# Kernel optimization log

Hardware: AMD Instinct MI355X
Metric: run time of the kernel (lower is better)

The kernel has to match this reference:

```python
import jax, jax.numpy as jnp
import numpy as np

VOCAB = 50000; EMBED = 300; KDIM = 128; KNUM = 21; KSIZES = (1, 2, 3)
B = 32; QLEN = 32; DLEN = 1024


def _kernel_mus(n):
    mus = [1.0]
    bs = 2.0 / (n - 1)
    mus.append(1.0 - bs / 2)
    for i in range(1, n - 1):
        mus.append(mus[i] - bs)
    return np.asarray(mus, np.float32)


def _kernel_sigmas(n):
    return np.asarray([0.001] + [0.1] * (n - 1), np.float32)


def setup_inputs() -> dict:
    key = jax.random.key(0)
    ks = jax.random.split(key, 12)
    inp = {
        'query_ids': jax.random.randint(ks[0], (B, QLEN), 0, VOCAB),
        'query_masks': jnp.ones((B, QLEN), jnp.float32),
        'doc_ids': jax.random.randint(ks[1], (B, DLEN), 0, VOCAB),
        'doc_masks': jnp.ones((B, DLEN), jnp.float32),
        'emb': jax.random.normal(ks[2], (VOCAB, EMBED), jnp.float32) * 0.02,
    }
    for i, k in enumerate(KSIZES):
        inp[f'conv_w{i+1}'] = jax.random.normal(ks[3 + i], (KDIM, EMBED, k), jnp.float32) / np.sqrt(EMBED * k)
        inp[f'conv_b{i+1}'] = jnp.zeros((KDIM,), jnp.float32)
    feat = KNUM * len(KSIZES) ** 2  # 189
    inp['dense_w'] = jax.random.normal(ks[9], (feat, 1), jnp.float32) * 0.05
    inp['dense_b'] = jnp.zeros((1,), jnp.float32)
    return inp


def _conv_relu(x, w, b):
    # x: [B, L, E], w: [O, E, K] -> [B, L-K+1, O] (VALID conv, matches torch Conv1d no padding)
    y = jax.lax.conv_general_dilated(x, w, (1,), 'VALID', dimension_numbers=('NWC', 'OIW', 'NWC'))
    return jax.nn.relu(y + b)


def _matcher(k_enc, k_mask, v_enc, v_mask, mus, sig):
    kn = k_enc / (jnp.linalg.norm(k_enc, axis=-1, keepdims=True) + 1e-13)
    vn = v_enc / (jnp.linalg.norm(v_enc, axis=-1, keepdims=True) + 1e-13)
    inter = jnp.einsum('bqd,bvd->bqv', kn, vn) * (k_mask[:, :, None] * v_mask[:, None, :])
    # multi-Gaussian soft-histogram over similarity: [B, q, v, KNUM]
    ko = jnp.exp(-((inter[..., None] - mus) ** 2) / (2.0 * sig ** 2))
    kde = jnp.log(jnp.maximum(ko.sum(axis=2), 1e-10)) * 0.01  # [B, q, KNUM]
    return (kde * k_mask[..., None]).sum(axis=1)  # [B, KNUM]


def reference(query_ids, query_masks, doc_ids, doc_masks, emb,
              conv_w1, conv_b1, conv_w2, conv_b2, conv_w3, conv_b3,
              dense_w, dense_b):
    mus = jnp.asarray(_kernel_mus(KNUM))
    sig = jnp.asarray(_kernel_sigmas(KNUM))
    qe = emb[query_ids]  # [B, QLEN, E]
    de = emb[doc_ids]    # [B, DLEN, E]
    cw = [(conv_w1, conv_b1), (conv_w2, conv_b2), (conv_w3, conv_b3)]
    q_encs = [_conv_relu(qe, w, b) for w, b in cw]
    d_encs = [_conv_relu(de, w, b) for w, b in cw]
    logits = jnp.concatenate([
        _matcher(q, query_masks[:, :q.shape[1]], d, doc_masks[:, :d.shape[1]], mus, sig)
        for q in q_encs for d in d_encs], axis=1)  # [B, 189]
    score = (logits @ dense_w + dense_b).squeeze(-1)  # [B]
    return score, logits
```

## Files before the change

### kernel.cpp

```cpp
#include <hip/hip_runtime.h>
#include <hip/hip_bf16.h>
#include <math.h>

#define NB 32
#define QL 32
#define DL 1024
#define EMB 300
#define EMBP 320
#define OD 128
#define KNUM 21
#define VOCAB 50000

typedef short short8 __attribute__((ext_vector_type(8)));
typedef float floatx4 __attribute__((ext_vector_type(4)));

static const size_t WP_OFF  = 0;
static const size_t DPK_OFF = 122880;
static const size_t QPK_OFF = 5365760;
static const size_t QH_OFF  = 5529920;
static const size_t QLO_OFF = 5726528;
static const size_t DH_OFF  = 5923136;
static const size_t DLO_OFF = 12214592;
static const size_t ACC_OFF = 18506048;
static const int ACC_SZ = 9 * NB * QL * KNUM;

#define QPLANE 131072
#define DPLANE 4194304

#define MROWS (NB * DL + NB * QL)
#define MTILES 264
#define CONV_BLOCKS (MTILES * 3)

#define PREPW_N 245760
#define GATHER_N ((MROWS + 2) * 40)

__device__ __constant__ int WPOFF_C[3] = {0, 40960, 122880};

__device__ __forceinline__ void gl_lds16(const ushort* g, char* l) {
    __builtin_amdgcn_global_load_lds(
        (const __attribute__((address_space(1))) unsigned int*)(g),
        (__attribute__((address_space(3))) unsigned int*)(l), 16, 0, 0);
}

__device__ __forceinline__ ushort bf16_bits(float f) {
    __hip_bfloat16 h = __float2bfloat16(f);
    return *reinterpret_cast<ushort*>(&h);
}

__global__ void gather_prep(const float* __restrict__ emb,
                            const int* __restrict__ dids, const int* __restrict__ qids,
                            const float* __restrict__ w1, const float* __restrict__ w2,
                            const float* __restrict__ w3,
                            ushort* __restrict__ dpk, ushort* __restrict__ qpk,
                            ushort* __restrict__ wp) {
    int idx = blockIdx.x * 256 + threadIdx.x;
    if (idx < PREPW_N) {
        const float* src;
        int k, rel, base;
        if (idx < 40960)        { k = 1; rel = idx;          src = w1; base = 0; }
        else if (idx < 122880)  { k = 2; rel = idx - 40960;  src = w2; base = 40960; }
        else                    { k = 3; rel = idx - 122880; src = w3; base = 122880; }
        int kd = 320 * k;
        int o = rel / kd;
        int jc = rel - o * kd;
        int j = jc / EMBP;
        int c = jc - j * EMBP;
        float f = (c < EMB) ? src[(o * EMB + c) * k + j] : 0.f;
        wp[base + rel] = bf16_bits(f);
        return;
    }
    idx -= PREPW_N;
    if (idx >= GATHER_N) return;
    const int DROWS = NB * DL;
    int r = idx / 40;
    int c0 = (idx - r * 40) * 8;
    int rid;
    ushort* dst;
    if (r < DROWS) { rid = dids[r]; dst = dpk + (size_t)r * EMBP; }
    else if (r < DROWS + NB * QL) { rid = qids[r - DROWS]; dst = qpk + (size_t)(r - DROWS) * EMBP; }
    else {
        uint4 zz = {0u, 0u, 0u, 0u};
        *reinterpret_cast<uint4*>(qpk + (size_t)(r - DROWS) * EMBP + c0) = zz;
        return;
    }
    const float* erow = emb + (size_t)rid * EMB;
    ushort v[8];
    if (c0 + 8 <= EMB) {
        float4 f0 = *reinterpret_cast<const float4*>(erow + c0);
        float4 f1 = *reinterpret_cast<const float4*>(erow + c0 + 4);
        float fv[8] = {f0.x, f0.y, f0.z, f0.w, f1.x, f1.y, f1.z, f1.w};
#pragma unroll
        for (int i = 0; i < 8; ++i) v[i] = bf16_bits(fv[i]);
    } else {
#pragma unroll
        for (int i = 0; i < 8; ++i) {
            int c = c0 + i;
            v[i] = bf16_bits((c < EMB) ? erow[c] : 0.f);
        }
    }
    *reinterpret_cast<uint4*>(dst + c0) = *reinterpret_cast<uint4*>(v);
}

__global__ __launch_bounds__(256) void conv_mfma(const ushort* __restrict__ xpk,
                                                 const float* __restrict__ dmask,
                                                 const float* __restrict__ qmask,
                                                 const ushort* __restrict__ wp,
                                                 const float* __restrict__ b1,
                                                 const float* __restrict__ b2,
                                                 const float* __restrict__ b3,
                                                 ushort* __restrict__ dh,
                                                 ushort* __restrict__ dlo,
                                                 ushort* __restrict__ qh,
                                                 ushort* __restrict__ qlo) {
    __shared__ __align__(16) char smem[2][33024];

    const int tid = threadIdx.x;
    const int bid = blockIdx.x;
    const int swz = (bid & 7) * (CONV_BLOCKS / 8) + (bid >> 3);
    const int z = swz % 3;
    const int tile = swz / 3;
    const int l0 = tile * 128;

    const int Kdim = EMBP * (z + 1);
    const int nk = 5 * (z + 1);
    const ushort* wpk = wp + WPOFF_C[z];
    const float* bias = (z == 0) ? b1 : ((z == 1) ? b2 : b3);

    const int wave = tid >> 6;
    const int lane = tid & 63;
    const int l15 = lane & 15;
    const int quad = lane >> 4;
    const int wm = wave >> 1;
    const int wn = wave & 1;

    const int srow = lane >> 3;
    const int scolx = (((lane & 7) ^ (lane >> 3) ^ 0) & 7) * 8;
    const ushort* a0 = xpk + (size_t)(l0 + wave * 8 + srow) * EMBP + scolx;
    const ushort* at = xpk + (size_t)(l0 + 128 + srow) * EMBP + scolx;
    const ushort* b0 = wpk + (size_t)(wave * 8 + srow) * Kdim + scolx;

    auto stage = [&](int buf, int kk) {
        int jj = (kk >= 10) ? 2 : ((kk >= 5) ? 1 : 0);
        int coff = (kk - jj * 5) * 64;
        int koff = kk * 64;
        char* abuf = smem[buf];
        char* bbuf = smem[buf] + 16640;
#pragma unroll
        for (int p = 0; p < 4; ++p)
            gl_lds16(a0 + p * (32 * EMBP) + coff, abuf + p * 4096 + wave * 1024);
        if (wave == 0 && lane < 16)
            gl_lds16(at + coff, abuf + 16384);
#pragma unroll
        for (int p = 0; p < 4; ++p)
            gl_lds16(b0 + (size_t)p * 32 * Kdim + koff, bbuf + p * 4096 + wave * 1024);
    };

    floatx4 acc[4][4];
#pragma unroll
    for (int i = 0; i < 4; ++i)
#pragma unroll
        for (int j = 0; j < 4; ++j) acc[i][j] = (floatx4)0.f;

    stage(0, 0);
    __syncthreads();

    int jjc = 0, ccc = 0;
    int buf = 0;
    for (int kk = 0; kk < nk; ++kk) {
        if (kk + 1 < nk) stage(buf ^ 1, kk + 1);
        const char* Ab = smem[buf];
        const char* Bb = smem[buf] + 16640;
        short8 af[2][4], bf[2][4];
#pragma unroll
        for (int h = 0; h < 2; ++h)
#pragma unroll
            for (int i = 0; i < 4; ++i) {
                int ra = wm * 64 + i * 16 + l15 + jjc;
                int rb = wn * 64 + i * 16 + l15;
                af[h][i] = *reinterpret_cast<const short8*>(
                    Ab + ra * 128 + ((((h << 2) | quad) ^ (ra & 7)) << 4));
                bf[h][i] = *reinterpret_cast<const short8*>(
                    Bb + rb * 128 + ((((h << 2) | quad) ^ (rb & 7)) << 4));
            }
#pragma unroll
        for (int h = 0; h < 2; ++h)
#pragma unroll
            for (int i = 0; i < 4; ++i)
#pragma unroll
                for (int j = 0; j < 4; ++j)
                    acc[i][j] = __builtin_amdgcn_mfma_f32_16x16x32_bf16(af[h][i], bf[h][j], acc[i][j], 0, 0, 0);
        ++ccc;
        if (ccc == 5) { ccc = 0; ++jjc; }
        __syncthreads();
        buf ^= 1;
    }

    float (*rowsum)[128] = reinterpret_cast<float(*)[128]>(smem);
    float bv[4];
#pragma unroll
    for (int j = 0; j < 4; ++j) bv[j] = bias[wn * 64 + j * 16 + l15];
#pragma unroll
    for (int i = 0; i < 4; ++i)
#pragma unroll
        for (int r = 0; r < 4; ++r) {
            float p = 0.f;
#pragma unroll
            for (int j = 0; j < 4; ++j) {
                float y = fmaxf(acc[i][j][r] + bv[j], 0.f);
                acc[i][j][r] = y;
                p += y * y;
            }
#pragma unroll
            for (int m = 1; m < 16; m <<= 1) p += __shfl_xor(p, m, 64);
            if (l15 == 0) rowsum[wn][wm * 64 + i * 16 + quad * 4 + r] = p;
        }
    __syncthreads();

#pragma unroll
    for (int i = 0; i < 4; ++i) {
#pragma unroll
        for (int rr = 0; rr < 4; ++rr) {
            int rl = wm * 64 + i * 16 + quad * 4 + rr;
            int r = l0 + rl;
            float tot = rowsum[0][rl] + rowsum[1][rl];
            float mv;
            ushort* hp;
            ushort* lp;
            if (r < NB * DL) {
                int l = r & (DL - 1);
                if (l >= DL - z) continue;
                mv = dmask[r];
                size_t base = (size_t)z * DPLANE + (size_t)r * OD;
                hp = dh + base; lp = dlo + base;
            } else {
                int t = r - NB * DL;
                int l = t & (QL - 1);
                if (l >= QL - z) continue;
                mv = qmask[t];
                size_t base = (size_t)z * QPLANE + (size_t)t * OD;
                hp = qh + base; lp = qlo + base;
            }
            float sc = mv / (sqrtf(tot) + 1e-13f);
            int cb = wn * 64 + l15;
#pragma unroll
            for (int j = 0; j < 4; ++j) {
                float v = acc[i][j][rr] * sc;
                __hip_bfloat16 h = __float2bfloat16(v);
                float hf = __bfloat162float(h);
                hp[cb + j * 16] = *reinterpret_cast<ushort*>(&h);
                __hip_bfloat16 l = __float2bfloat16(v - hf);
                lp[cb + j * 16] = *reinterpret_cast<ushort*>(&l);
            }
        }
    }
}

__global__ __launch_bounds__(256, 4) void matcher_kernel(const ushort* __restrict__ qh_g,
                                                         const ushort* __restrict__ ql_g,
                                                         const ushort* __restrict__ vh_g,
                                                         const ushort* __restrict__ vl_g,
                                                         float* __restrict__ accb) {
    __shared__ __align__(16) float Sm[32 * 132];
    __shared__ float stageb[672];

    const int tid = threadIdx.x;
    const int pp = blockIdx.z;
    const int b = blockIdx.y;
    const int v0 = blockIdx.x * 128;
    const int qi = pp / 3;
    const int di = pp - qi * 3;
    const int Vk = 1024 - di;

    const ushort* qhb = qh_g + (size_t)qi * QPLANE + (size_t)b * (QL * OD);
    const ushort* qlb = ql_g + (size_t)qi * QPLANE + (size_t)b * (QL * OD);
    const ushort* vhb = vh_g + (size_t)di * DPLANE + (size_t)b * (DL * OD) + (size_t)v0 * OD;
    const ushort* vlb = vl_g + (size_t)di * DPLANE + (size_t)b * (DL * OD) + (size_t)v0 * OD;

    const int wave = tid >> 6;
    const int lane = tid & 63;
    const int l15 = lane & 15;
    const int quad = lane >> 4;

    floatx4 acc[2][2];
#pragma unroll
    for (int i = 0; i < 2; ++i)
#pragma unroll
        for (int j = 0; j < 2; ++j) acc[i][j] = (floatx4)0.f;

#pragma unroll
    for (int kw = 0; kw < 4; ++kw) {
        const int ko = kw * 32 + quad * 8;
        short8 qh[2], ql[2], vh[2], vl[2];
#pragma unroll
        for (int i = 0; i < 2; ++i) {
            const int qr = i * 16 + l15;
            const int vr = wave * 32 + i * 16 + l15;
            qh[i] = *reinterpret_cast<const short8*>(qhb + qr * OD + ko);
            ql[i] = *reinterpret_cast<const short8*>(qlb + qr * OD + ko);
            vh[i] = *reinterpret_cast<const short8*>(vhb + (size_t)vr * OD + ko);
            vl[i] = *reinterpret_cast<const short8*>(vlb + (size_t)vr * OD + ko);
        }
#pragma unroll
        for (int i = 0; i < 2; ++i)
#pragma unroll
            for (int j = 0; j < 2; ++j) {
                acc[i][j] = __builtin_amdgcn_mfma_f32_16x16x32_bf16(qh[i], vh[j], acc[i][j], 0, 0, 0);
                acc[i][j] = __builtin_amdgcn_mfma_f32_16x16x32_bf16(qh[i], vl[j], acc[i][j], 0, 0, 0);
                acc[i][j] = __builtin_amdgcn_mfma_f32_16x16x32_bf16(ql[i], vh[j], acc[i][j], 0, 0, 0);
            }
    }

    const int vmax = min(128, Vk - v0);
#pragma unroll
    for (int i = 0; i < 2; ++i)
#pragma unroll
        for (int j = 0; j < 2; ++j)
#pragma unroll
            for (int r = 0; r < 4; ++r) {
                int q = i * 16 + quad * 4 + r;
                int v = wave * 32 + j * 16 + l15;
                float val = acc[i][j][r];
                if (v >= vmax) val = 1.0e4f;
                Sm[q * 132 + v] = val;
            }
    __syncthreads();

    {
        const int q = tid >> 3;
        const int c = tid & 7;
        const float* srow = &Sm[q * 132 + c * 16];
        const float Am  = -72.13475204f;
        const float Am5 = -14.426950408f;
        const float A0  = -721347.52f;
        const float C   = 0x1.0p-126f;

        float s00 = 0.f, s01 = 0.f, s02 = 0.f, s03 = 0.f, s04 = 0.f, s05 = 0.f,
              s06 = 0.f, s07 = 0.f, s08 = 0.f, s09 = 0.f, s10 = 0.f, s11 = 0.f,
              s12 = 0.f, s13 = 0.f, s14 = 0.f, s15 = 0.f, s16 = 0.f, s17 = 0.f,
              s18 = 0.f, s19 = 0.f, s20 = 0.f;

#define GACC(B) { B = __builtin_fmaf(tx, C, B); B = __builtin_fmaf(ty, C, B); \
                  B = __builtin_fmaf(tz, C, B); B = __builtin_fmaf(tw, C, B); }
#define GSTEP(B, g) { tx *= Rx * (g); ty *= Ry * (g); tz *= Rz * (g); tw *= Rw * (g); GACC(B) }

#pragma unroll
        for (int jj = 0; jj < 4; ++jj) {
            float4 s4 = *reinterpret_cast<const float4*>(srow + jj * 4);
            float dx = s4.x - 0.95f, dy = s4.y - 0.95f, dz = s4.z - 0.95f, dwv = s4.w - 0.95f;
            float tx = __builtin_exp2f(__builtin_fmaf(Am * dx, dx, 126.f));
            float ty = __builtin_exp2f(__builtin_fmaf(Am * dy, dy, 126.f));
            float tz = __builtin_exp2f(__builtin_fmaf(Am * dz, dz, 126.f));
            float tw = __builtin_exp2f(__builtin_fmaf(Am * dwv, dwv, 126.f));
            float Rx = __builtin_exp2f(Am5 * dx);
            float Ry = __builtin_exp2f(Am5 * dy);
            float Rz = __builtin_exp2f(Am5 * dz);
            float Rw = __builtin_exp2f(Am5 * dwv);
            GACC(s01)
            GSTEP(s02, 6.0653066e-01f) GSTEP(s03, 2.2313016e-01f)
            GSTEP(s04, 8.2084999e-02f) GSTEP(s05, 3.0197383e-02f)
            GSTEP(s06, 1.1108997e-02f) GSTEP(s07, 4.0867714e-03f)
            GSTEP(s08, 1.5034391e-03f) GSTEP(s09, 5.5308438e-04f)
            GSTEP(s10, 2.0346837e-04f) GSTEP(s11, 7.4851830e-05f)
            GSTEP(s12, 2.7536450e-05f) GSTEP(s13, 1.0130095e-05f)
            GSTEP(s14, 3.7266532e-06f) GSTEP(s15, 1.3709590e-06f)
            GSTEP(s16, 5.0434766e-07f) GSTEP(s17, 1.8553914e-07f)
            GSTEP(s18, 6.8256033e-08f) GSTEP(s19, 2.5110699e-08f)
            GSTEP(s20, 9.2374496e-09f)
            float ex = s4.x - 1.f, ey = s4.y - 1.f, ez = s4.z - 1.f, ew = s4.w - 1.f;
            s00 += __builtin_exp2f((A0 * ex) * ex);
            s00 += __builtin_exp2f((A0 * ey) * ey);
            s00 += __builtin_exp2f((A0 * ez) * ez);
            s00 += __builtin_exp2f((A0 * ew) * ew);
        }
#undef GSTEP
#undef GACC

#define GRED(B) { B += __shfl_xor(B, 1, 64); B += __shfl_xor(B, 2, 64); B += __shfl_xor(B, 4, 64); }
        GRED(s00) GRED(s01) GRED(s02) GRED(s03) GRED(s04) GRED(s05) GRED(s06)
        GRED(s07) GRED(s08) GRED(s09) GRED(s10) GRED(s11) GRED(s12) GRED(s13)
        GRED(s14) GRED(s15) GRED(s16) GRED(s17) GRED(s18) GRED(s19) GRED(s20)
#undef GRED
        if (c == 0) {
            float* sp = &stageb[q * KNUM];
            sp[0]  = s00; sp[1]  = s01; sp[2]  = s02; sp[3]  = s03; sp[4]  = s04;
            sp[5]  = s05; sp[6]  = s06; sp[7]  = s07; sp[8]  = s08; sp[9]  = s09;
            sp[10] = s10; sp[11] = s11; sp[12] = s12; sp[13] = s13; sp[14] = s14;
            sp[15] = s15; sp[16] = s16; sp[17] = s17; sp[18] = s18; sp[19] = s19;
            sp[20] = s20;
        }
    }
    __syncthreads();

    {
        float* dst = &accb[((size_t)(pp * NB + b) * QL) * KNUM];
        for (int i = tid; i < 32 * KNUM; i += 256)
            atomicAdd(dst + i, stageb[i]);
    }
}

__global__ void finalize_kernel(const float* __restrict__ accb,
                                const float* __restrict__ qmask,
                                const float* __restrict__ dw,
                                const float* __restrict__ db,
                                float* __restrict__ out) {
    __shared__ float prod[192];
    int b = blockIdx.x;
    int tid = threadIdx.x;
    if (tid < 189) {
        int pq = tid / 21;
        int t = tid - pq * 21;
        int qi = pq / 3;
        int Qk = 32 - qi;
        const float* ab = accb + ((pq * NB + b) * QL) * KNUM + t;
        float s = 0.f;
        for (int q = 0; q < Qk; ++q)
            s += logf(fmaxf(ab[q * KNUM], 1e-10f)) * qmask[b * QL + q];
        float lg = s * 0.01f;
        out[NB + b * 189 + tid] = lg;
        prod[tid] = lg * dw[tid];
    }
    __syncthreads();
    if (tid == 0) {
        float sc = db[0];
        for (int i = 0; i < 189; ++i) sc += prod[i];
        out[b] = sc;
    }
}

extern "C" void kernel_launch(void* const* d_in, const int* in_sizes, int n_in,
                              void* d_out, int out_size, void* d_ws, size_t ws_size,
                              hipStream_t stream) {
    const int* qids = (const int*)d_in[0];
    const float* qmask = (const float*)d_in[1];
    const int* dids = (const int*)d_in[2];
    const float* dmask = (const float*)d_in[3];
    const float* emb = (const float*)d_in[4];
    const float* w1 = (const float*)d_in[5];
    const float* b1 = (const float*)d_in[6];
    const float* w2 = (const float*)d_in[7];
    const float* b2 = (const float*)d_in[8];
    const float* w3 = (const float*)d_in[9];
    const float* b3 = (const float*)d_in[10];
    const float* dw = (const float*)d_in[11];
    const float* db = (const float*)d_in[12];
    float* out = (float*)d_out;
    float* ws = (float*)d_ws;

    ushort* wp  = (ushort*)(ws + WP_OFF);
    ushort* dpk = (ushort*)(ws + DPK_OFF);
    ushort* qpk = (ushort*)(ws + QPK_OFF);
    ushort* qh  = (ushort*)(ws + QH_OFF);
    ushort* qlo = (ushort*)(ws + QLO_OFF);
    ushort* dh  = (ushort*)(ws + DH_OFF);
    ushort* dlo = (ushort*)(ws + DLO_OFF);
    float* accb = ws + ACC_OFF;

    hipMemsetAsync(accb, 0, ACC_SZ * sizeof(float), stream);
    gather_prep<<<(PREPW_N + GATHER_N + 255) / 256, 256, 0, stream>>>(
        emb, dids, qids, w1, w2, w3, dpk, qpk, wp);

    conv_mfma<<<CONV_BLOCKS, 256, 0, stream>>>(dpk, dmask, qmask, wp, b1, b2, b3, dh, dlo, qh, qlo);

    matcher_kernel<<<dim3(8, NB, 9), 256, 0, stream>>>(qh, qlo, dh, dlo, accb);
    finalize_kernel<<<NB, 256, 0, stream>>>(accb, qmask, dw, db, out);
}
```

Measured before the change: 220.4 us.

## Reuse doc tile across all three query encodings in one matcher block

The matcher grid's z dimension now covers only the three doc encodings, and each block loops over the three query encodings. The doc high/low bf16 fragments are loaded once per k-step and reused for the MFMA against all three query planes, cutting global doc traffic to a third. The cost is three times the accumulator registers, serialized Gaussian-histogram passes inside each block, and a third as many blocks, which may reduce parallelism and latency hiding. A redundant XOR term in the conv swizzle is also removed.

```diff
diff --git a/kernel.cpp b/kernel.cpp
--- a/kernel.cpp
+++ b/kernel.cpp
@@ -134,7 +134,7 @@
     const int wn = wave & 1;
 
     const int srow = lane >> 3;
-    const int scolx = (((lane & 7) ^ (lane >> 3) ^ 0) & 7) * 8;
+    const int scolx = (((lane & 7) ^ (lane >> 3)) & 7) * 8;
     const ushort* a0 = xpk + (size_t)(l0 + wave * 8 + srow) * EMBP + scolx;
     const ushort* at = xpk + (size_t)(l0 + 128 + srow) * EMBP + scolx;
     const ushort* b0 = wpk + (size_t)(wave * 8 + srow) * Kdim + scolx;
@@ -264,15 +264,13 @@
     __shared__ float stageb[672];
 
     const int tid = threadIdx.x;
-    const int pp = blockIdx.z;
+    const int di = blockIdx.z;
     const int b = blockIdx.y;
     const int v0 = blockIdx.x * 128;
-    const int qi = pp / 3;
-    const int di = pp - qi * 3;
     const int Vk = 1024 - di;
 
-    const ushort* qhb = qh_g + (size_t)qi * QPLANE + (size_t)b * (QL * OD);
-    const ushort* qlb = ql_g + (size_t)qi * QPLANE + (size_t)b * (QL * OD);
+    const ushort* qhB = qh_g + (size_t)b * (QL * OD);
+    const ushort* qlB = ql_g + (size_t)b * (QL * OD);
     const ushort* vhb = vh_g + (size_t)di * DPLANE + (size_t)b * (DL * OD) + (size_t)v0 * OD;
     const ushort* vlb = vl_g + (size_t)di * DPLANE + (size_t)b * (DL * OD) + (size_t)v0 * OD;
 
@@ -281,120 +279,133 @@
     const int l15 = lane & 15;
     const int quad = lane >> 4;
 
-    floatx4 acc[2][2];
-#pragma unroll
-    for (int i = 0; i < 2; ++i)
-#pragma unroll
-        for (int j = 0; j < 2; ++j) acc[i][j] = (floatx4)0.f;
+    floatx4 acc[3][2][2];
+#pragma unroll
+    for (int qi = 0; qi < 3; ++qi)
+#pragma unroll
+        for (int i = 0; i < 2; ++i)
+#pragma unroll
+            for (int j = 0; j < 2; ++j) acc[qi][i][j] = (floatx4)0.f;
 
 #pragma unroll
     for (int kw = 0; kw < 4; ++kw) {
         const int ko = kw * 32 + quad * 8;
-        short8 qh[2], ql[2], vh[2], vl[2];
+        short8 vh[2], vl[2];
 #pragma unroll
         for (int i = 0; i < 2; ++i) {
-            const int qr = i * 16 + l15;
             const int vr = wave * 32 + i * 16 + l15;
-            qh[i] = *reinterpret_cast<const short8*>(qhb + qr * OD + ko);
-            ql[i] = *reinterpret_cast<const short8*>(qlb + qr * OD + ko);
             vh[i] = *reinterpret_cast<const short8*>(vhb + (size_t)vr * OD + ko);
             vl[i] = *reinterpret_cast<const short8*>(vlb + (size_t)vr * OD + ko);
         }
 #pragma unroll
+        for (int qi = 0; qi < 3; ++qi) {
+            short8 qh[2], ql[2];
+#pragma unroll
+            for (int i = 0; i < 2; ++i) {
+                const int qr = i * 16 + l15;
+                qh[i] = *reinterpret_cast<const short8*>(qhB + qi * QPLANE + qr * OD + ko);
+                ql[i] = *reinterpret_cast<const short8*>(qlB + qi * QPLANE + qr * OD + ko);
+            }
+#pragma unroll
+            for (int i = 0; i < 2; ++i)
+#pragma unroll
+                for (int j = 0; j < 2; ++j) {
+                    acc[qi][i][j] = __builtin_amdgcn_mfma_f32_16x16x32_bf16(qh[i], vh[j], acc[qi][i][j], 0, 0, 0);
+                    acc[qi][i][j] = __builtin_amdgcn_mfma_f32_16x16x32_bf16(qh[i], vl[j], acc[qi][i][j], 0, 0, 0);
+                    acc[qi][i][j] = __builtin_amdgcn_mfma_f32_16x16x32_bf16(ql[i], vh[j], acc[qi][i][j], 0, 0, 0);
+                }
+        }
+    }
+
+    const int vmax = min(128, Vk - v0);
+
+#pragma unroll
+    for (int qi = 0; qi < 3; ++qi) {
+#pragma unroll
         for (int i = 0; i < 2; ++i)
 #pragma unroll
-            for (int j = 0; j < 2; ++j) {
-                acc[i][j] = __builtin_amdgcn_mfma_f32_16x16x32_bf16(qh[i], vh[j], acc[i][j], 0, 0, 0);
-                acc[i][j] = __builtin_amdgcn_mfma_f32_16x16x32_bf16(qh[i], vl[j], acc[i][j], 0, 0, 0);
-                acc[i][j] = __builtin_amdgcn_mfma_f32_16x16x32_bf16(ql[i], vh[j], acc[i][j], 0, 0, 0);
-            }
-    }
-
-    const int vmax = min(128, Vk - v0);
-#pragma unroll
-    for (int i = 0; i < 2; ++i)
-#pragma unroll
-        for (int j = 0; j < 2; ++j)
-#pragma unroll
-            for (int r = 0; r < 4; ++r) {
-                int q = i * 16 + quad * 4 + r;
-                int v = wave * 32 + j * 16 + l15;
-                float val = acc[i][j][r];
-                if (v >= vmax) val = 1.0e4f;
-                Sm[q * 132 + v] = val;
-            }
-    __syncthreads();
-
-    {
-        const int q = tid >> 3;
-        const int c = tid & 7;
-        const float* srow = &Sm[q * 132 + c * 16];
-        const float Am  = -72.13475204f;
-        const float Am5 = -14.426950408f;
-        const float A0  = -721347.52f;
-        const float C   = 0x1.0p-126f;
-
-        float s00 = 0.f, s01 = 0.f, s02 = 0.f, s03 = 0.f, s04 = 0.f, s05 = 0.f,
-              s06 = 0.f, s07 = 0.f, s08 = 0.f, s09 = 0.f, s10 = 0.f, s11 = 0.f,
-              s12 = 0.f, s13 = 0.f, s14 = 0.f, s15 = 0.f, s16 = 0.f, s17 = 0.f,
-              s18 = 0.f, s19 = 0.f, s20 = 0.f;
+            for (int j = 0; j < 2; ++j)
+#pragma unroll
+                for (int r = 0; r < 4; ++r) {
+                    int q = i * 16 + quad * 4 + r;
+                    int v = wave * 32 + j * 16 + l15;
+                    float val = acc[qi][i][j][r];
+                    if (v >= vmax) val = 1.0e4f;
+                    Sm[q * 132 + v] = val;
+                }
+        __syncthreads();
+
+        {
+            const int q = tid >> 3;
+            const int c = tid & 7;
+            const float* srow = &Sm[q * 132 + c * 16];
+            const float Am  = -72.13475204f;
+            const float Am5 = -14.426950408f;
+            const float A0  = -721347.52f;
+            const float C   = 0x1.0p-126f;
+
+            float s00 = 0.f, s01 = 0.f, s02 = 0.f, s03 = 0.f, s04 = 0.f, s05 = 0.f,
+                  s06 = 0.f, s07 = 0.f, s08 = 0.f, s09 = 0.f, s10 = 0.f, s11 = 0.f,
+                  s12 = 0.f, s13 = 0.f, s14 = 0.f, s15 = 0.f, s16 = 0.f, s17 = 0.f,
+                  s18 = 0.f, s19 = 0.f, s20 = 0.f;
 
 #define GACC(B) { B = __builtin_fmaf(tx, C, B); B = __builtin_fmaf(ty, C, B); \
                   B = __builtin_fmaf(tz, C, B); B = __builtin_fmaf(tw, C, B); }
 #define GSTEP(B, g) { tx *= Rx * (g); ty *= Ry * (g); tz *= Rz * (g); tw *= Rw * (g); GACC(B) }
 
 #pragma unroll
-        for (int jj = 0; jj < 4; ++jj) {
-            float4 s4 = *reinterpret_cast<const float4*>(srow + jj * 4);
-            float dx = s4.x - 0.95f, dy = s4.y - 0.95f, dz = s4.z - 0.95f, dwv = s4.w - 0.95f;
-            float tx = __builtin_exp2f(__builtin_fmaf(Am * dx, dx, 126.f));
-            float ty = __builtin_exp2f(__builtin_fmaf(Am * dy, dy, 126.f));
-            float tz = __builtin_exp2f(__builtin_fmaf(Am * dz, dz, 126.f));
-            float tw = __builtin_exp2f(__builtin_fmaf(Am * dwv, dwv, 126.f));
-            float Rx = __builtin_exp2f(Am5 * dx);
-            float Ry = __builtin_exp2f(Am5 * dy);
-            float Rz = __builtin_exp2f(Am5 * dz);
-            float Rw = __builtin_exp2f(Am5 * dwv);
-            GACC(s01)
-            GSTEP(s02, 6.0653066e-01f) GSTEP(s03, 2.2313016e-01f)
-            GSTEP(s04, 8.2084999e-02f) GSTEP(s05, 3.0197383e-02f)
-            GSTEP(s06, 1.1108997e-02f) GSTEP(s07, 4.0867714e-03f)
-            GSTEP(s08, 1.5034391e-03f) GSTEP(s09, 5.5308438e-04f)
-            GSTEP(s10, 2.0346837e-04f) GSTEP(s11, 7.4851830e-05f)
-            GSTEP(s12, 2.7536450e-05f) GSTEP(s13, 1.0130095e-05f)
-            GSTEP(s14, 3.7266532e-06f) GSTEP(s15, 1.3709590e-06f)
-            GSTEP(s16, 5.0434766e-07f) GSTEP(s17, 1.8553914e-07f)
-            GSTEP(s18, 6.8256033e-08f) GSTEP(s19, 2.5110699e-08f)
-            GSTEP(s20, 9.2374496e-09f)
-            float ex = s4.x - 1.f, ey = s4.y - 1.f, ez = s4.z - 1.f, ew = s4.w - 1.f;
-            s00 += __builtin_exp2f((A0 * ex) * ex);
-            s00 += __builtin_exp2f((A0 * ey) * ey);
-            s00 += __builtin_exp2f((A0 * ez) * ez);
-            s00 += __builtin_exp2f((A0 * ew) * ew);
-        }
+            for (int jj = 0; jj < 4; ++jj) {
+                float4 s4 = *reinterpret_cast<const float4*>(srow + jj * 4);
+                float dx = s4.x - 0.95f, dy = s4.y - 0.95f, dz = s4.z - 0.95f, dwv = s4.w - 0.95f;
+                float tx = __builtin_exp2f(__builtin_fmaf(Am * dx, dx, 126.f));
+                float ty = __builtin_exp2f(__builtin_fmaf(Am * dy, dy, 126.f));
+                float tz = __builtin_exp2f(__builtin_fmaf(Am * dz, dz, 126.f));
+                float tw = __builtin_exp2f(__builtin_fmaf(Am * dwv, dwv, 126.f));
+                float Rx = __builtin_exp2f(Am5 * dx);
+                float Ry = __builtin_exp2f(Am5 * dy);
+                float Rz = __builtin_exp2f(Am5 * dz);
+                float Rw = __builtin_exp2f(Am5 * dwv);
+                GACC(s01)
+                GSTEP(s02, 6.0653066e-01f) GSTEP(s03, 2.2313016e-01f)
+                GSTEP(s04, 8.2084999e-02f) GSTEP(s05, 3.0197383e-02f)
+                GSTEP(s06, 1.1108997e-02f) GSTEP(s07, 4.0867714e-03f)
+                GSTEP(s08, 1.5034391e-03f) GSTEP(s09, 5.5308438e-04f)
+                GSTEP(s10, 2.0346837e-04f) GSTEP(s11, 7.4851830e-05f)
+                GSTEP(s12, 2.7536450e-05f) GSTEP(s13, 1.0130095e-05f)
+                GSTEP(s14, 3.7266532e-06f) GSTEP(s15, 1.3709590e-06f)
+                GSTEP(s16, 5.0434766e-07f) GSTEP(s17, 1.8553914e-07f)
+                GSTEP(s18, 6.8256033e-08f) GSTEP(s19, 2.5110699e-08f)
+                GSTEP(s20, 9.2374496e-09f)
+                float ex = s4.x - 1.f, ey = s4.y - 1.f, ez = s4.z - 1.f, ew = s4.w - 1.f;
+                s00 += __builtin_exp2f((A0 * ex) * ex);
+                s00 += __builtin_exp2f((A0 * ey) * ey);
+                s00 += __builtin_exp2f((A0 * ez) * ez);
+                s00 += __builtin_exp2f((A0 * ew) * ew);
+            }
 #undef GSTEP
 #undef GACC
 
 #define GRED(B) { B += __shfl_xor(B, 1, 64); B += __shfl_xor(B, 2, 64); B += __shfl_xor(B, 4, 64); }
-        GRED(s00) GRED(s01) GRED(s02) GRED(s03) GRED(s04) GRED(s05) GRED(s06)
-        GRED(s07) GRED(s08) GRED(s09) GRED(s10) GRED(s11) GRED(s12) GRED(s13)
-        GRED(s14) GRED(s15) GRED(s16) GRED(s17) GRED(s18) GRED(s19) GRED(s20)
+            GRED(s00) GRED(s01) GRED(s02) GRED(s03) GRED(s04) GRED(s05) GRED(s06)
+            GRED(s07) GRED(s08) GRED(s09) GRED(s10) GRED(s11) GRED(s12) GRED(s13)
+            GRED(s14) GRED(s15) GRED(s16) GRED(s17) GRED(s18) GRED(s19) GRED(s20)
 #undef GRED
-        if (c == 0) {
-            float* sp = &stageb[q * KNUM];
-            sp[0]  = s00; sp[1]  = s01; sp[2]  = s02; sp[3]  = s03; sp[4]  = s04;
-            sp[5]  = s05; sp[6]  = s06; sp[7]  = s07; sp[8]  = s08; sp[9]  = s09;
-            sp[10] = s10; sp[11] = s11; sp[12] = s12; sp[13] = s13; sp[14] = s14;
-            sp[15] = s15; sp[16] = s16; sp[17] = s17; sp[18] = s18; sp[19] = s19;
-            sp[20] = s20;
-        }
-    }
-    __syncthreads();
-
-    {
-        float* dst = &accb[((size_t)(pp * NB + b) * QL) * KNUM];
-        for (int i = tid; i < 32 * KNUM; i += 256)
-            atomicAdd(dst + i, stageb[i]);
+            if (c == 0) {
+                float* sp = &stageb[q * KNUM];
+                sp[0]  = s00; sp[1]  = s01; sp[2]  = s02; sp[3]  = s03; sp[4]  = s04;
+                sp[5]  = s05; sp[6]  = s06; sp[7]  = s07; sp[8]  = s08; sp[9]  = s09;
+                sp[10] = s10; sp[11] = s11; sp[12] = s12; sp[13] = s13; sp[14] = s14;
+                sp[15] = s15; sp[16] = s16; sp[17] = s17; sp[18] = s18; sp[19] = s19;
+                sp[20] = s20;
+            }
+        }
+        __syncthreads();
+
+        {
+            float* dst = &accb[((size_t)((qi * 3 + di) * NB + b) * QL) * KNUM];
+            for (int i = tid; i < 32 * KNUM; i += 256)
+                atomicAdd(dst + i, stageb[i]);
+        }
     }
 }
 
@@ -461,6 +472,6 @@
 
     conv_mfma<<<CONV_BLOCKS, 256, 0, stream>>>(dpk, dmask, qmask, wp, b1, b2, b3, dh, dlo, qh, qlo);
 
-    matcher_kernel<<<dim3(8, NB, 9), 256, 0, stream>>>(qh, qlo, dh, dlo, accb);
+    matcher_kernel<<<dim3(8, NB, 3), 256, 0, stream>>>(qh, qlo, dh, dlo, accb);
     finalize_kernel<<<NB, 256, 0, stream>>>(accb, qmask, dw, db, out);
 }
```

After: 233.7 us. 6.1% more time.
